# Performance work log

Hardware: AMD Instinct MI355X
Metric: run time of the kernel (lower is better)

## Reference

```python
import jax, jax.numpy as jnp
import numpy as np
from jax import lax

DEC = [256, 128, 64, 32]
INS = [512, 256, 128, 64]


def _conv2d(x, w, b, pad):
    y = lax.conv_general_dilated(x, w, (1, 1), [(pad, pad), (pad, pad)],
                                 dimension_numbers=('NCHW', 'OIHW', 'NCHW'))
    return y + b[None, :, None, None]


def _conv_transpose2d(x, w_t, b):
    # torch ConvTranspose2d(k=3, stride=2, padding=1, output_padding=1): H -> 2H
    # equivalent to lhs-dilated conv with spatially flipped, IO-transposed kernel
    w = jnp.flip(jnp.transpose(w_t, (1, 0, 2, 3)), (2, 3))  # [out, in, 3, 3]
    y = lax.conv_general_dilated(x, w, (1, 1), [(1, 2), (1, 2)],
                                 lhs_dilation=(2, 2),
                                 dimension_numbers=('NCHW', 'OIHW', 'NCHW'))
    return y + b[None, :, None, None]


def setup_inputs() -> dict:
    key = jax.random.key(0)
    ks = iter(jax.random.split(key, 40))
    d = {}
    d['enc_feat'] = jax.random.normal(next(ks), (8, 512, 16, 16), jnp.float32)
    d['semantic_map'] = jax.random.normal(next(ks), (8, 32, 256, 256), jnp.float32)

    def w(k, shape, fan_in):
        return jax.random.normal(k, shape, jnp.float32) / np.float32(np.sqrt(fan_in))

    for i in range(4):
        d['wt%d' % i] = w(next(ks), (INS[i], DEC[i], 3, 3), INS[i] * 9)  # torch convT layout [in,out,kh,kw]
        d['bt%d' % i] = jnp.zeros((DEC[i],), jnp.float32)
        d['wc%d' % i] = w(next(ks), (DEC[i], DEC[i], 3, 3), DEC[i] * 9)
        d['bc%d' % i] = jnp.zeros((DEC[i],), jnp.float32)
    d['w_attn'] = w(next(ks), (16, 32, 1, 1), 32)
    d['b_attn'] = jnp.zeros((16,), jnp.float32)
    d['w_fin'] = w(next(ks), (1, 16, 1, 1), 16)
    d['b_fin'] = jnp.zeros((1,), jnp.float32)
    return d


def _forward(enc_feat, semantic_map, wts, bts, wcs, bcs, w_attn, b_attn, w_fin, b_fin):
    x = enc_feat
    for i in range(4):
        x = jax.nn.elu(_conv_transpose2d(x, wts[i], bts[i]))
        x = jax.nn.elu(_conv2d(x, wcs[i], bcs[i], 1))
        # skip concats are zero-channel in the only executable config -> identity
    # DynamicSemanticAttention (channel attention over C' = in_ch // 2)
    q = _conv2d(x, w_attn, b_attn, 0)                 # [B, 16, H, W]
    kf = _conv2d(semantic_map, w_attn, b_attn, 0)     # [B, 16, H, W]
    B, C, H, W = q.shape
    qf = q.reshape(B, C, H * W)                        # [B, C', N]
    attn = jnp.einsum('bcn,bdn->bcd', qf, kf.reshape(B, C, H * W))  # [B, C', C']
    attn = jax.nn.softmax(attn, axis=-1)
    fused = jnp.einsum('bcd,bdn->bcn', attn, qf).reshape(B, C, H, W) + q
    return jax.nn.sigmoid(_conv2d(fused, w_fin, b_fin, 0))  # [B, 1, H, W]


def reference(enc_feat, semantic_map, wt0, bt0, wc0, bc0, wt1, bt1, wc1, bc1,
              wt2, bt2, wc2, bc2, wt3, bt3, wc3, bc3, w_attn, b_attn, w_fin, b_fin):
    wts = [wt0, wt1, wt2, wt3]
    bts = [bt0, bt1, bt2, bt3]
    wcs = [wc0, wc1, wc2, wc3]
    bcs = [bc0, bc1, bc2, bc3]
    return _forward(enc_feat, semantic_map, wts, bts, wcs, bcs,
                    w_attn, b_attn, w_fin, b_fin)
```

## Files before the change

### kernel.cpp

```cpp
#include <hip/hip_runtime.h>
#include <hip/hip_bf16.h>
#include <math.h>

typedef _Float16 f16;
typedef _Float16 h8 __attribute__((ext_vector_type(8)));
typedef _Float16 h4 __attribute__((ext_vector_type(4)));
typedef float    f4 __attribute__((ext_vector_type(4)));

__device__ __forceinline__ float elu_f(float v) { return v > 0.f ? v : __expf(v) - 1.f; }
__device__ __forceinline__ float sigmoid_f(float v) { return 1.f / (1.f + __expf(-v)); }

struct PrepDesc { const float* src; unsigned dstOff; int OC; int IC; int tr; };
struct P8 { PrepDesc d[8]; };

__global__ void prep_all_k(P8 p, f16* __restrict__ wp,
                           const float* __restrict__ enc, f16* __restrict__ enc_cl) {
    __shared__ float ts[32][257];
    if (blockIdx.x < 128) {
        const int b = blockIdx.x >> 4, cg = blockIdx.x & 15;
        const int tid = threadIdx.x;
        #pragma unroll
        for (int i = 0; i < 32; ++i)
            ts[i][tid] = enc[((size_t)(b * 512 + cg * 32 + i)) * 256 + tid];
        __syncthreads();
        #pragma unroll
        for (int k = 0; k < 4; ++k) {
            h8 v;
            #pragma unroll
            for (int q = 0; q < 8; ++q) v[q] = (f16)ts[k * 8 + q][tid];
            *(h8*)(enc_cl + ((size_t)(b * 256 + tid)) * 512 + cg * 32 + k * 8) = v;
        }
        return;
    }
    unsigned idx = (blockIdx.x - 128) * 256u + threadIdx.x;
    for (int s = 0; s < 8; ++s) {
        const int IC = p.d[s].IC, OC = p.d[s].OC;
        const unsigned cnt = (unsigned)(OC * 9 * IC);
        if (idx < cnt) {
            const int nicc = IC >> 5;
            const int j    = idx & 7;
            const int lane = (idx >> 3) & 63;
            const int mt   = (idx >> 9) & 1;
            unsigned r = idx >> 10;
            const int tap = r % 9;  r /= 9;
            const int icchunk = r % nicc;
            const int ocg     = r / nicc;
            const int oc = ocg * 32 + mt * 16 + (lane & 15);
            const int ic = icchunk * 32 + (lane >> 4) * 8 + j;
            const float v = p.d[s].tr ? p.d[s].src[((size_t)ic * OC + oc) * 9 + tap]
                                      : p.d[s].src[((size_t)oc * IC + ic) * 9 + tap];
            wp[p.d[s].dstOff + idx] = (f16)v;
            return;
        }
        idx -= cnt;
    }
}

template<int SKS>
__device__ __forceinline__ h8 stage_elem(const f16* __restrict__ in, size_t off,
                                         size_t srcTot, const float* __restrict__ sbias,
                                         int ch0) {
    if constexpr (SKS == 1) {
        return *(const h8*)(in + off);
    } else {
        float s[8];
        const h8 t0 = *(const h8*)(in + off);
        #pragma unroll
        for (int j = 0; j < 8; ++j) s[j] = (float)t0[j];
        #pragma unroll
        for (int k = 1; k < SKS; ++k) {
            const h8 tk = *(const h8*)(in + (size_t)k * srcTot + off);
            #pragma unroll
            for (int j = 0; j < 8; ++j) s[j] += (float)tk[j];
        }
        const float4 b0 = *(const float4*)(sbias + ch0);
        const float4 b1 = *(const float4*)(sbias + ch0 + 4);
        h8 v;
        v[0] = (f16)elu_f(s[0] + b0.x); v[1] = (f16)elu_f(s[1] + b0.y);
        v[2] = (f16)elu_f(s[2] + b0.z); v[3] = (f16)elu_f(s[3] + b0.w);
        v[4] = (f16)elu_f(s[4] + b1.x); v[5] = (f16)elu_f(s[5] + b1.y);
        v[6] = (f16)elu_f(s[6] + b1.z); v[7] = (f16)elu_f(s[7] + b1.w);
        return v;
    }
}

template<int C, int H, int W, int HT, int WT, int NWN, int KS, int SKS>
__launch_bounds__(256, 2)
__global__ void conv3_mfma(const f16* __restrict__ in, const f16* __restrict__ wp,
                           const float* __restrict__ bias, const float* __restrict__ sbias,
                           size_t srcTot, f16* __restrict__ out, f16* __restrict__ pout) {
    constexpr int NWR = 4 / NWN;
    constexpr int RH  = HT / NWR;
    constexpr int PIXR = WT + 2;
    constexpr int ROWS = HT + 2;
    constexpr int XB = ROWS * PIXR * 80;
    constexpr int NICC = C / 32;
    constexpr int XTILES = W / WT;
    __shared__ __align__(16) char xlds[XB];

    const int tid = threadIdx.x;
    const int wid = tid >> 6, lane = tid & 63;
    const int ln15 = lane & 15, lg = lane >> 4;
    const int ni = wid % NWN, ri = wid / NWN;
    const int bz = blockIdx.z;
    const int bb = bz / (C / 32), ocg = bz % (C / 32);
    const int oc0 = ocg * 32;
    const int bx = blockIdx.x;
    const int xt = bx % XTILES, ks = bx / XTILES;
    const int h0 = blockIdx.y * HT, w0 = xt * WT;
    const int colb = ni * 16 + ln15;

    f4 acc[RH][2] = {};

    for (int icc = ks * (C / KS); icc < (ks + 1) * (C / KS); icc += 32) {
        __syncthreads();
        for (int t = tid; t < ROWS * PIXR * 4; t += 256) {
            const int g = t & 3, pix = t >> 2;
            const int rr = pix / PIXR, ww = pix - rr * PIXR;
            const int gh = h0 - 1 + rr, gw = w0 - 1 + ww;
            h8 v = {};
            if (gh >= 0 && gh < H && gw >= 0 && gw < W) {
                const size_t off = (((size_t)bb * H + gh) * W + gw) * C + icc + g * 8;
                v = stage_elem<SKS>(in, off, srcTot, sbias, icc + g * 8);
            }
            *(h8*)(xlds + pix * 80 + g * 16) = v;
        }
        __syncthreads();

        const f16* wbl = wp + ((size_t)(ocg * NICC + (icc >> 5)) * 18) * 512 + lane * 8;
        #pragma unroll
        for (int dw = 0; dw < 3; ++dw) {
            h8 afd[3][2];
            #pragma unroll
            for (int dh = 0; dh < 3; ++dh)
                #pragma unroll
                for (int mt = 0; mt < 2; ++mt)
                    afd[dh][mt] = *(const h8*)(wbl + ((dh * 3 + dw) * 2 + mt) * 512);
            h8 bfv[RH + 2];
            #pragma unroll
            for (int q = 0; q < RH + 2; ++q)
                bfv[q] = *(const h8*)(xlds + ((ri * RH + q) * PIXR + colb + dw) * 80 + lg * 16);
            #pragma unroll
            for (int r = 0; r < RH; ++r) {
                #pragma unroll
                for (int dh = 0; dh < 3; ++dh) {
                    acc[r][0] = __builtin_amdgcn_mfma_f32_16x16x32_f16(afd[dh][0], bfv[r + dh], acc[r][0], 0, 0, 0);
                    acc[r][1] = __builtin_amdgcn_mfma_f32_16x16x32_f16(afd[dh][1], bfv[r + dh], acc[r][1], 0, 0, 0);
                }
            }
        }
    }

    #pragma unroll
    for (int r = 0; r < RH; ++r) {
        const int oh = h0 + ri * RH + r;
        const int ow = w0 + colb;
        #pragma unroll
        for (int mt = 0; mt < 2; ++mt) {
            const int ocl = mt * 16 + lg * 4;
            const f4 v = acc[r][mt];
            if constexpr (KS > 1) {
                const size_t TOT = (size_t)8 * H * W * C;
                h4 hv = {(f16)v.x, (f16)v.y, (f16)v.z, (f16)v.w};
                *(h4*)(pout + (size_t)ks * TOT +
                       (((size_t)bb * H + oh) * W + ow) * C + oc0 + ocl) = hv;
            } else {
                const float4 b4 = *(const float4*)(bias + oc0 + ocl);
                h4 hv = {(f16)elu_f(v.x + b4.x), (f16)elu_f(v.y + b4.y),
                         (f16)elu_f(v.z + b4.z), (f16)elu_f(v.w + b4.w)};
                *(h4*)(out + (((size_t)bb * H + oh) * W + ow) * C + oc0 + ocl) = hv;
            }
        }
    }
}

template<int IC, int OC, int Hi, int Wi, int KS, int SKS>
__launch_bounds__(256, 2)
__global__ void convt_mfma(const f16* __restrict__ in, const f16* __restrict__ wp,
                           const float* __restrict__ bias, const float* __restrict__ sbias,
                           size_t srcTot, f16* __restrict__ out, f16* __restrict__ pout) {
    constexpr int HT = 4, WT = 16;
    constexpr int PIXR = WT + 1;
    constexpr int ROWS = HT + 1;
    constexpr int XB = ROWS * PIXR * 80;
    constexpr int NICC = IC / 32;
    constexpr int XTILES = Wi / WT;
    __shared__ __align__(16) char xlds[XB];

    const int tid = threadIdx.x;
    const int wid = tid >> 6, lane = tid & 63;
    const int ln15 = lane & 15, lg = lane >> 4;
    const int iloc = wid;
    const int bz = blockIdx.z;
    const int bb = bz / (OC / 32), ocg = bz % (OC / 32);
    const int oc0 = ocg * 32;
    const int bx = blockIdx.x;
    const int xt = bx % XTILES, ks = bx / XTILES;
    const int i0 = blockIdx.y * HT, j0 = xt * WT;

    f4 acc[4][2] = {};

    for (int icc = ks * (IC / KS); icc < (ks + 1) * (IC / KS); icc += 32) {
        __syncthreads();
        for (int t = tid; t < ROWS * PIXR * 4; t += 256) {
            const int g = t & 3, pix = t >> 2;
            const int rr = pix / PIXR, ww = pix - rr * PIXR;
            const int gh = i0 + rr, gw = j0 + ww;
            h8 v = {};
            if (gh < Hi && gw < Wi) {
                const size_t off = (((size_t)bb * Hi + gh) * Wi + gw) * IC + icc + g * 8;
                v = stage_elem<SKS>(in, off, srcTot, sbias, icc + g * 8);
            }
            *(h8*)(xlds + pix * 80 + g * 16) = v;
        }
        __syncthreads();

        const f16* wbl = wp + ((size_t)(ocg * NICC + (icc >> 5)) * 18) * 512 + lane * 8;
        h8 af[9][2];
        #pragma unroll
        for (int tap = 0; tap < 9; ++tap)
            #pragma unroll
            for (int mt = 0; mt < 2; ++mt)
                af[tap][mt] = *(const h8*)(wbl + (tap * 2 + mt) * 512);

        h8 bf[2][2];
        #pragma unroll
        for (int a = 0; a < 2; ++a)
            #pragma unroll
            for (int b = 0; b < 2; ++b)
                bf[a][b] = *(const h8*)(xlds + ((iloc + a) * PIXR + ln15 + b) * 80 + lg * 16);

        #pragma unroll
        for (int p = 0; p < 4; ++p) {
            const int di = p >> 1, dj = p & 1;
            #pragma unroll
            for (int a = 0; a < 2; ++a) {
                if (a > di) continue;
                const int kh = 1 + di - 2 * a;
                #pragma unroll
                for (int b = 0; b < 2; ++b) {
                    if (b > dj) continue;
                    const int kw = 1 + dj - 2 * b;
                    const int tap = kh * 3 + kw;
                    acc[p][0] = __builtin_amdgcn_mfma_f32_16x16x32_f16(af[tap][0], bf[a][b], acc[p][0], 0, 0, 0);
                    acc[p][1] = __builtin_amdgcn_mfma_f32_16x16x32_f16(af[tap][1], bf[a][b], acc[p][1], 0, 0, 0);
                }
            }
        }
    }

    #pragma unroll
    for (int p = 0; p < 4; ++p) {
        const int orow = 2 * (i0 + iloc) + (p >> 1);
        const int ocol = 2 * (j0 + ln15) + (p & 1);
        #pragma unroll
        for (int mt = 0; mt < 2; ++mt) {
            const int ocl = mt * 16 + lg * 4;
            const f4 v = acc[p][mt];
            if constexpr (KS > 1) {
                const size_t TOT = (size_t)8 * (2 * Hi) * (2 * Wi) * OC;
                h4 hv = {(f16)v.x, (f16)v.y, (f16)v.z, (f16)v.w};
                *(h4*)(pout + (size_t)ks * TOT +
                       (((size_t)bb * (2 * Hi) + orow) * (2 * Wi) + ocol) * OC + oc0 + ocl) = hv;
            } else {
                const float4 b4 = *(const float4*)(bias + oc0 + ocl);
                h4 hv = {(f16)elu_f(v.x + b4.x), (f16)elu_f(v.y + b4.y),
                         (f16)elu_f(v.z + b4.z), (f16)elu_f(v.w + b4.w)};
                *(h4*)(out + (((size_t)bb * (2 * Hi) + orow) * (2 * Wi) + ocol) * OC + oc0 + ocl) = hv;
            }
        }
    }
}

#define KCH 128
__launch_bounds__(256)
__global__ void gram_mfma_k(const f16* __restrict__ x3, const float* __restrict__ sem,
                            float* __restrict__ part, float* __restrict__ sums) {
    __shared__ __align__(16) f16 xs[4][32][66];
    __shared__ float pl[4][1024];
    __shared__ float sl[4][64];
    const int b = blockIdx.y, kc = blockIdx.x;
    const int tid = threadIdx.x, wid = tid >> 6, lane = tid & 63;
    const int row = lane & 15, kg = lane >> 4;
    const size_t N = 65536;
    const int p0 = kc * 512 + wid * 128;

    const float* sb = sem + ((size_t)b * 32 + row) * N + p0 + kg * 8;
    const int spx = lane >> 1, shalf = lane & 1;

    f4 acc00 = {}, acc01 = {}, acc10 = {}, acc11 = {};
    float sx0 = 0.f, sx1 = 0.f, ss0 = 0.f, ss1 = 0.f;

    for (int s = 0; s < 4; ++s) {
        const f16* xp = x3 + ((size_t)b * N + p0 + s * 32 + spx) * 32 + shalf * 16;
        const h8 w0 = *(const h8*)xp;
        const h8 w1 = *(const h8*)(xp + 8);
        const float4 f0 = *(const float4*)(sb + s * 32);
        const float4 f1 = *(const float4*)(sb + s * 32 + 4);
        const float4 g0 = *(const float4*)(sb + 16 * N + s * 32);
        const float4 g1 = *(const float4*)(sb + 16 * N + s * 32 + 4);
        *(h8*)&xs[wid][spx][shalf * 16]     = w0;
        *(h8*)&xs[wid][spx][shalf * 16 + 8] = w1;
        h8 a0, a1;
        #pragma unroll
        for (int j = 0; j < 8; ++j) {
            a0[j] = xs[wid][kg * 8 + j][row];
            a1[j] = xs[wid][kg * 8 + j][row + 16];
        }
        const h8 b0 = {(f16)f0.x, (f16)f0.y, (f16)f0.z, (f16)f0.w,
                       (f16)f1.x, (f16)f1.y, (f16)f1.z, (f16)f1.w};
        const h8 b1 = {(f16)g0.x, (f16)g0.y, (f16)g0.z, (f16)g0.w,
                       (f16)g1.x, (f16)g1.y, (f16)g1.z, (f16)g1.w};
        acc00 = __builtin_amdgcn_mfma_f32_16x16x32_f16(a0, b0, acc00, 0, 0, 0);
        acc01 = __builtin_amdgcn_mfma_f32_16x16x32_f16(a0, b1, acc01, 0, 0, 0);
        acc10 = __builtin_amdgcn_mfma_f32_16x16x32_f16(a1, b0, acc10, 0, 0, 0);
        acc11 = __builtin_amdgcn_mfma_f32_16x16x32_f16(a1, b1, acc11, 0, 0, 0);
        #pragma unroll
        for (int q = 0; q < 8; ++q) { sx0 += (float)a0[q]; sx1 += (float)a1[q]; }
        ss0 += (f0.x + f0.y + f0.z + f0.w) + (f1.x + f1.y + f1.z + f1.w);
        ss1 += (g0.x + g0.y + g0.z + g0.w) + (g1.x + g1.y + g1.z + g1.w);
    }

    sx0 += __shfl_xor(sx0, 16); sx0 += __shfl_xor(sx0, 32);
    sx1 += __shfl_xor(sx1, 16); sx1 += __shfl_xor(sx1, 32);
    ss0 += __shfl_xor(ss0, 16); ss0 += __shfl_xor(ss0, 32);
    ss1 += __shfl_xor(ss1, 16); ss1 += __shfl_xor(ss1, 32);

    #pragma unroll
    for (int reg = 0; reg < 4; ++reg) {
        const int c0 = 4 * kg + reg;
        pl[wid][c0 * 32 + row]               = acc00[reg];
        pl[wid][c0 * 32 + 16 + row]          = acc01[reg];
        pl[wid][(16 + c0) * 32 + row]        = acc10[reg];
        pl[wid][(16 + c0) * 32 + 16 + row]   = acc11[reg];
    }
    if (lane < 16) {
        sl[wid][row]      = sx0;
        sl[wid][16 + row] = sx1;
        sl[wid][32 + row] = ss0;
        sl[wid][48 + row] = ss1;
    }
    __syncthreads();

    float* pb = part + ((size_t)b * KCH + kc) * 1024;
    #pragma unroll
    for (int t = tid; t < 1024; t += 256)
        pb[t] = pl[0][t] + pl[1][t] + pl[2][t] + pl[3][t];
    if (tid < 64)
        sums[((size_t)b * KCH + kc) * 64 + tid] = sl[0][tid] + sl[1][tid] + sl[2][tid] + sl[3][tid];
}

__launch_bounds__(256)
__global__ void gram_reduce_k(const float* __restrict__ part, const float* __restrict__ sums,
                              float* __restrict__ part2, float* __restrict__ sums2) {
    const int b = blockIdx.y, g = blockIdx.x;
    const int tid = threadIdx.x;
    const int i4 = tid * 4;
    f4 a = {};
    #pragma unroll 4
    for (int ch = 0; ch < 16; ++ch) {
        const f4 v = *(const f4*)(part + ((size_t)b * KCH + g * 16 + ch) * 1024 + i4);
        a.x += v.x; a.y += v.y; a.z += v.z; a.w += v.w;
    }
    *(f4*)(part2 + ((size_t)b * 8 + g) * 1024 + i4) = a;
    if (tid < 64) {
        float s = 0.f;
        #pragma unroll 4
        for (int ch = 0; ch < 16; ++ch) s += sums[((size_t)b * KCH + g * 16 + ch) * 64 + tid];
        sums2[((size_t)b * 8 + g) * 64 + tid] = s;
    }
}

__launch_bounds__(256)
__global__ void attn_finish_v3(const float* __restrict__ part, const float* __restrict__ sums,
                               const float* __restrict__ wa, const float* __restrict__ ba,
                               const float* __restrict__ wf, const float* __restrict__ bf,
                               float* __restrict__ u, float* __restrict__ cb) {
    __shared__ float G[32][33];
    __shared__ float T[16][33];
    __shared__ float A[16][17];
    __shared__ float Sx[32], Ss[32], px[16], ps[16], v[16];
    const int b = blockIdx.x, tid = threadIdx.x;

    float a4[4] = {0.f, 0.f, 0.f, 0.f};
    for (int p = 0; p < 8; ++p) {
        const float* pp = part + ((size_t)b * 8 + p) * 1024 + tid;
        a4[0] += pp[0]; a4[1] += pp[256]; a4[2] += pp[512]; a4[3] += pp[768];
    }
    #pragma unroll
    for (int q = 0; q < 4; ++q) {
        const int t = tid + q * 256;
        G[t >> 5][t & 31] = a4[q];
    }
    if (tid < 64) {
        float s = 0.f;
        for (int p = 0; p < 8; ++p) s += sums[((size_t)b * 8 + p) * 64 + tid];
        if (tid < 32) Sx[tid] = s; else Ss[tid - 32] = s;
    }
    __syncthreads();
    for (int t = tid; t < 512; t += 256) {
        const int c = t >> 5, f = t & 31;
        float s = 0.f;
        #pragma unroll
        for (int e = 0; e < 32; ++e) s = fmaf(wa[c * 32 + e], G[e][f], s);
        T[c][f] = s;
    }
    if (tid < 32) {
        const int c = tid & 15;
        const float* S = (tid < 16) ? Sx : Ss;
        float s = 0.f;
        #pragma unroll
        for (int e = 0; e < 32; ++e) s = fmaf(wa[c * 32 + e], S[e], s);
        if (tid < 16) px[c] = s; else ps[c] = s;
    }
    __syncthreads();
    {
        const int c = tid >> 4, d = tid & 15;
        float s = 0.f;
        #pragma unroll
        for (int f2 = 0; f2 < 32; ++f2) s = fmaf(T[c][f2], wa[d * 32 + f2], s);
        s += px[c] * ba[d] + ba[c] * ps[d] + 65536.f * ba[c] * ba[d];
        A[c][d] = s;
    }
    __syncthreads();
    if (tid < 16) {
        float m = A[tid][0];
        #pragma unroll
        for (int d = 1; d < 16; ++d) m = fmaxf(m, A[tid][d]);
        float s = 0.f;
        #pragma unroll
        for (int d = 0; d < 16; ++d) { const float e = __expf(A[tid][d] - m); A[tid][d] = e; s += e; }
        const float inv = 1.f / s;
        #pragma unroll
        for (int d = 0; d < 16; ++d) A[tid][d] *= inv;
    }
    __syncthreads();
    if (tid < 16) {
        float s = wf[tid];
        #pragma unroll
        for (int c = 0; c < 16; ++c) s = fmaf(wf[c], A[c][tid], s);
        v[tid] = s;
    }
    __syncthreads();
    if (tid < 32) {
        float s = 0.f;
        #pragma unroll
        for (int d = 0; d < 16; ++d) s = fmaf(v[d], wa[d * 32 + tid], s);
        u[b * 32 + tid] = s;
    }
    if (tid == 0) {
        float s2 = bf[0];
        #pragma unroll
        for (int d = 0; d < 16; ++d) s2 = fmaf(v[d], ba[d], s2);
        cb[b] = s2;
    }
}

__launch_bounds__(256)
__global__ void final_k(const f16* __restrict__ x3, const float* __restrict__ u,
                        const float* __restrict__ cb, float* __restrict__ out) {
    const int b = blockIdx.y;
    const int nn = blockIdx.x * 256 + threadIdx.x;
    const f16* xb = x3 + ((size_t)b * 65536 + nn) * 32;
    const float* ub = u + b * 32;
    float acc = cb[b];
    #pragma unroll
    for (int g = 0; g < 4; ++g) {
        const h8 v = *(const h8*)(xb + g * 8);
        #pragma unroll
        for (int q = 0; q < 8; ++q) acc = fmaf(ub[g * 8 + q], (float)v[q], acc);
    }
    out[(size_t)b * 65536 + nn] = sigmoid_f(acc);
}

extern "C" void kernel_launch(void* const* d_in, const int* in_sizes, int n_in,
                              void* d_out, int out_size, void* d_ws, size_t ws_size,
                              hipStream_t stream) {
    const float* enc   = (const float*)d_in[0];
    const float* sem   = (const float*)d_in[1];
    const float* wt0   = (const float*)d_in[2];
    const float* bt0   = (const float*)d_in[3];
    const float* wc0   = (const float*)d_in[4];
    const float* bc0   = (const float*)d_in[5];
    const float* wt1   = (const float*)d_in[6];
    const float* bt1   = (const float*)d_in[7];
    const float* wc1   = (const float*)d_in[8];
    const float* bc1   = (const float*)d_in[9];
    const float* wt2   = (const float*)d_in[10];
    const float* bt2   = (const float*)d_in[11];
    const float* wc2   = (const float*)d_in[12];
    const float* bc2   = (const float*)d_in[13];
    const float* wt3   = (const float*)d_in[14];
    const float* bt3   = (const float*)d_in[15];
    const float* wc3   = (const float*)d_in[16];
    const float* bc3   = (const float*)d_in[17];
    const float* wattn = (const float*)d_in[18];
    const float* battn = (const float*)d_in[19];
    const float* wfin  = (const float*)d_in[20];
    const float* bfin  = (const float*)d_in[21];

    char* W = (char*)d_ws;
    f16*   actA   = (f16*)(W + 0);
    f16*   actB   = (f16*)(W + 33554432);
    f16*   x3cl   = (f16*)(W + 67108864);
    f16*   wp     = (f16*)(W + 100663296);
    f16*   enc_cl = (f16*)(W + 105906176);
    float* part   = (float*)(W + 108003328);
    float* sums   = (float*)(W + 112197632);
    float* part2  = (float*)(W + 112459776);
    float* sums2  = (float*)(W + 112721920);
    float* u      = (float*)(W + 112738304);
    float* cb     = (float*)(W + 112739328);
    float* out    = (float*)d_out;
    f16* pfA = actA;
    f16* pfB = actB;

    P8 p;
    p.d[0] = {wt0, 0u,       256, 512, 1};
    p.d[1] = {wc0, 1179648u, 256, 256, 0};
    p.d[2] = {wt1, 1769472u, 128, 256, 1};
    p.d[3] = {wc1, 2064384u, 128, 128, 0};
    p.d[4] = {wt2, 2211840u,  64, 128, 1};
    p.d[5] = {wc2, 2285568u,  64,  64, 0};
    p.d[6] = {wt3, 2322432u,  32,  64, 1};
    p.d[7] = {wc3, 2340864u,  32,  32, 0};
    prep_all_k<<<9308, 256, 0, stream>>>(p, wp, enc, enc_cl);

    convt_mfma<512, 256, 16, 16, 4, 1><<<dim3(4, 4, 64), 256, 0, stream>>>(
        enc_cl, wp, nullptr, nullptr, 0, nullptr, pfA);
    conv3_mfma<256, 32, 32, 8, 32, 2, 4, 4><<<dim3(4, 4, 64), 256, 0, stream>>>(
        pfA, wp + 1179648, nullptr, bt0, 2097152, nullptr, pfB);
    convt_mfma<256, 128, 32, 32, 2, 4><<<dim3(4, 8, 32), 256, 0, stream>>>(
        pfB, wp + 1769472, nullptr, bc0, 2097152, nullptr, pfA);
    conv3_mfma<128, 64, 64, 4, 64, 4, 2, 2><<<dim3(2, 16, 32), 256, 0, stream>>>(
        pfA, wp + 2064384, nullptr, bt1, 4194304, nullptr, pfB);
    convt_mfma<128, 64, 64, 64, 1, 2><<<dim3(4, 16, 16), 256, 0, stream>>>(
        pfB, wp + 2211840, bt2, bc1, 4194304, actA, nullptr);
    conv3_mfma<64, 128, 128, 4, 64, 4, 1, 1><<<dim3(2, 32, 16), 256, 0, stream>>>(
        actA, wp + 2285568, bc2, nullptr, 0, actB, nullptr);
    convt_mfma<64, 32, 128, 128, 1, 1><<<dim3(8, 32, 8), 256, 0, stream>>>(
        actB, wp + 2322432, bt3, nullptr, 0, actA, nullptr);
    conv3_mfma<32, 256, 256, 4, 64, 4, 1, 1><<<dim3(4, 64, 8), 256, 0, stream>>>(
        actA, wp + 2340864, bc3, nullptr, 0, x3cl, nullptr);

    gram_mfma_k<<<dim3(KCH, 8), 256, 0, stream>>>(x3cl, sem, part, sums);
    gram_reduce_k<<<dim3(8, 8), 256, 0, stream>>>(part, sums, part2, sums2);
    attn_finish_v3<<<8, 256, 0, stream>>>(part2, sums2, wattn, battn, wfin, bfin, u, cb);
    final_k<<<dim3(256, 8), 256, 0, stream>>>(x3cl, u, cb, out);
}
```

Baseline: 227.7 us.

## Fuse final conv3 with gram accumulation and retune early decoder split-K

The last 3x3 conv (32 channels, 256x256) now also computes the per-tile gram partials and row sums against the semantic map, using the freshly computed activations kept in LDS. This removes the separate gram kernel and its reread of x3 from global memory. The partial count doubles to 256 chunks per batch, so the reduce kernel reads more data. The early decoder stages also get new conv3/convt template parameters and split-K factors, and the bias/ELU epilogues move to different stages.

Result: no change. 228.7 us (+0.4%).

```diff
diff --git a/kernel.cpp b/kernel.cpp
--- a/kernel.cpp
+++ b/kernel.cpp
@@ -272,53 +272,116 @@
     }
 }
 
-#define KCH 128
-__launch_bounds__(256)
-__global__ void gram_mfma_k(const f16* __restrict__ x3, const float* __restrict__ sem,
-                            float* __restrict__ part, float* __restrict__ sums) {
-    __shared__ __align__(16) f16 xs[4][32][66];
-    __shared__ float pl[4][1024];
-    __shared__ float sl[4][64];
-    const int b = blockIdx.y, kc = blockIdx.x;
-    const int tid = threadIdx.x, wid = tid >> 6, lane = tid & 63;
-    const int row = lane & 15, kg = lane >> 4;
+__launch_bounds__(256, 2)
+__global__ void conv3_gram_k(const f16* __restrict__ in, const f16* __restrict__ wp,
+                             const float* __restrict__ bias, const float* __restrict__ sem,
+                             f16* __restrict__ out, float* __restrict__ part,
+                             float* __restrict__ sums) {
+    constexpr int C = 32, H = 256, W = 256, HT = 4, WT = 64;
+    constexpr int PIXR = WT + 2;
+    constexpr int ROWS = HT + 2;
+    constexpr int XB = ROWS * PIXR * 80;
+    constexpr int X3B = 32 * 264 * 2;
+    constexpr int LDSB = X3B + 16384 + 1024;
+    __shared__ __align__(16) char lds[(XB > LDSB) ? XB : LDSB];
+    char* xlds = lds;
+    f16*   x3l = (f16*)lds;
+    float* pl  = (float*)(lds + X3B);
+    float* sl  = (float*)(lds + X3B + 16384);
+
+    const int tid = threadIdx.x;
+    const int wid = tid >> 6, lane = tid & 63;
+    const int ln15 = lane & 15, lg = lane >> 4;
+    const int ni = wid;
+    const int bb = blockIdx.z;
+    const int h0 = blockIdx.y * HT, w0 = blockIdx.x * WT;
+    const int colb = ni * 16 + ln15;
+
+    f4 acc[4][2] = {};
+
+    for (int t = tid; t < ROWS * PIXR * 4; t += 256) {
+        const int g = t & 3, pix = t >> 2;
+        const int rr = pix / PIXR, ww = pix - rr * PIXR;
+        const int gh = h0 - 1 + rr, gw = w0 - 1 + ww;
+        h8 v = {};
+        if (gh >= 0 && gh < H && gw >= 0 && gw < W)
+            v = *(const h8*)(in + (((size_t)bb * H + gh) * W + gw) * C + g * 8);
+        *(h8*)(xlds + pix * 80 + g * 16) = v;
+    }
+    __syncthreads();
+
+    const f16* wbl = wp + lane * 8;
+    #pragma unroll
+    for (int dw = 0; dw < 3; ++dw) {
+        h8 afd[3][2];
+        #pragma unroll
+        for (int dh = 0; dh < 3; ++dh)
+            #pragma unroll
+            for (int mt = 0; mt < 2; ++mt)
+                afd[dh][mt] = *(const h8*)(wbl + ((dh * 3 + dw) * 2 + mt) * 512);
+        h8 bfv[6];
+        #pragma unroll
+        for (int q = 0; q < 6; ++q)
+            bfv[q] = *(const h8*)(xlds + (q * PIXR + colb + dw) * 80 + lg * 16);
+        #pragma unroll
+        for (int r = 0; r < 4; ++r) {
+            #pragma unroll
+            for (int dh = 0; dh < 3; ++dh) {
+                acc[r][0] = __builtin_amdgcn_mfma_f32_16x16x32_f16(afd[dh][0], bfv[r + dh], acc[r][0], 0, 0, 0);
+                acc[r][1] = __builtin_amdgcn_mfma_f32_16x16x32_f16(afd[dh][1], bfv[r + dh], acc[r][1], 0, 0, 0);
+            }
+        }
+    }
+    __syncthreads();
+
+    #pragma unroll
+    for (int r = 0; r < 4; ++r) {
+        const int oh = h0 + r, ow = w0 + colb;
+        const int px = r * 64 + colb;
+        #pragma unroll
+        for (int mt = 0; mt < 2; ++mt) {
+            const int ocl = mt * 16 + lg * 4;
+            const float4 b4 = *(const float4*)(bias + ocl);
+            const f4 v = acc[r][mt];
+            h4 hv = {(f16)elu_f(v.x + b4.x), (f16)elu_f(v.y + b4.y),
+                     (f16)elu_f(v.z + b4.z), (f16)elu_f(v.w + b4.w)};
+            *(h4*)(out + (((size_t)bb * H + oh) * W + ow) * C + ocl) = hv;
+            x3l[(ocl + 0) * 264 + px] = hv[0];
+            x3l[(ocl + 1) * 264 + px] = hv[1];
+            x3l[(ocl + 2) * 264 + px] = hv[2];
+            x3l[(ocl + 3) * 264 + px] = hv[3];
+        }
+    }
+    __syncthreads();
+
+    const int row = ln15, kg = lg;
     const size_t N = 65536;
-    const int p0 = kc * 512 + wid * 128;
-
-    const float* sb = sem + ((size_t)b * 32 + row) * N + p0 + kg * 8;
-    const int spx = lane >> 1, shalf = lane & 1;
-
-    f4 acc00 = {}, acc01 = {}, acc10 = {}, acc11 = {};
+    const float* sb = sem + ((size_t)bb * 32 + row) * N + (size_t)(h0 + wid) * 256 + w0 + kg * 8;
+
+    f4 g00 = {}, g01 = {}, g10 = {}, g11 = {};
     float sx0 = 0.f, sx1 = 0.f, ss0 = 0.f, ss1 = 0.f;
 
-    for (int s = 0; s < 4; ++s) {
-        const f16* xp = x3 + ((size_t)b * N + p0 + s * 32 + spx) * 32 + shalf * 16;
-        const h8 w0 = *(const h8*)xp;
-        const h8 w1 = *(const h8*)(xp + 8);
-        const float4 f0 = *(const float4*)(sb + s * 32);
-        const float4 f1 = *(const float4*)(sb + s * 32 + 4);
-        const float4 g0 = *(const float4*)(sb + 16 * N + s * 32);
-        const float4 g1 = *(const float4*)(sb + 16 * N + s * 32 + 4);
-        *(h8*)&xs[wid][spx][shalf * 16]     = w0;
-        *(h8*)&xs[wid][spx][shalf * 16 + 8] = w1;
-        h8 a0, a1;
-        #pragma unroll
-        for (int j = 0; j < 8; ++j) {
-            a0[j] = xs[wid][kg * 8 + j][row];
-            a1[j] = xs[wid][kg * 8 + j][row + 16];
-        }
+    #pragma unroll
+    for (int ks = 0; ks < 2; ++ks) {
+        const int k0 = ks * 32;
+        const h8 a0 = *(const h8*)(x3l + row * 264 + wid * 64 + k0 + kg * 8);
+        const h8 a1 = *(const h8*)(x3l + (row + 16) * 264 + wid * 64 + k0 + kg * 8);
+        const float4 f0 = *(const float4*)(sb + k0);
+        const float4 f1 = *(const float4*)(sb + k0 + 4);
+        const float4 q0 = *(const float4*)(sb + 16 * N + k0);
+        const float4 q1 = *(const float4*)(sb + 16 * N + k0 + 4);
         const h8 b0 = {(f16)f0.x, (f16)f0.y, (f16)f0.z, (f16)f0.w,
                        (f16)f1.x, (f16)f1.y, (f16)f1.z, (f16)f1.w};
-        const h8 b1 = {(f16)g0.x, (f16)g0.y, (f16)g0.z, (f16)g0.w,
-                       (f16)g1.x, (f16)g1.y, (f16)g1.z, (f16)g1.w};
-        acc00 = __builtin_amdgcn_mfma_f32_16x16x32_f16(a0, b0, acc00, 0, 0, 0);
-        acc01 = __builtin_amdgcn_mfma_f32_16x16x32_f16(a0, b1, acc01, 0, 0, 0);
-        acc10 = __builtin_amdgcn_mfma_f32_16x16x32_f16(a1, b0, acc10, 0, 0, 0);
-        acc11 = __builtin_amdgcn_mfma_f32_16x16x32_f16(a1, b1, acc11, 0, 0, 0);
+        const h8 b1 = {(f16)q0.x, (f16)q0.y, (f16)q0.z, (f16)q0.w,
+                       (f16)q1.x, (f16)q1.y, (f16)q1.z, (f16)q1.w};
+        g00 = __builtin_amdgcn_mfma_f32_16x16x32_f16(a0, b0, g00, 0, 0, 0);
+        g01 = __builtin_amdgcn_mfma_f32_16x16x32_f16(a0, b1, g01, 0, 0, 0);
+        g10 = __builtin_amdgcn_mfma_f32_16x16x32_f16(a1, b0, g10, 0, 0, 0);
+        g11 = __builtin_amdgcn_mfma_f32_16x16x32_f16(a1, b1, g11, 0, 0, 0);
         #pragma unroll
         for (int q = 0; q < 8; ++q) { sx0 += (float)a0[q]; sx1 += (float)a1[q]; }
         ss0 += (f0.x + f0.y + f0.z + f0.w) + (f1.x + f1.y + f1.z + f1.w);
-        ss1 += (g0.x + g0.y + g0.z + g0.w) + (g1.x + g1.y + g1.z + g1.w);
+        ss1 += (q0.x + q0.y + q0.z + q0.w) + (q1.x + q1.y + q1.z + q1.w);
     }
 
     sx0 += __shfl_xor(sx0, 16); sx0 += __shfl_xor(sx0, 32);
@@ -329,25 +392,25 @@
     #pragma unroll
     for (int reg = 0; reg < 4; ++reg) {
         const int c0 = 4 * kg + reg;
-        pl[wid][c0 * 32 + row]               = acc00[reg];
-        pl[wid][c0 * 32 + 16 + row]          = acc01[reg];
-        pl[wid][(16 + c0) * 32 + row]        = acc10[reg];
-        pl[wid][(16 + c0) * 32 + 16 + row]   = acc11[reg];
+        pl[wid * 1024 + c0 * 32 + row]             = g00[reg];
+        pl[wid * 1024 + c0 * 32 + 16 + row]        = g01[reg];
+        pl[wid * 1024 + (16 + c0) * 32 + row]      = g10[reg];
+        pl[wid * 1024 + (16 + c0) * 32 + 16 + row] = g11[reg];
     }
     if (lane < 16) {
-        sl[wid][row]      = sx0;
-        sl[wid][16 + row] = sx1;
-        sl[wid][32 + row] = ss0;
-        sl[wid][48 + row] = ss1;
-    }
-    __syncthreads();
-
-    float* pb = part + ((size_t)b * KCH + kc) * 1024;
-    #pragma unroll
+        sl[wid * 64 + row]      = sx0;
+        sl[wid * 64 + 16 + row] = sx1;
+        sl[wid * 64 + 32 + row] = ss0;
+        sl[wid * 64 + 48 + row] = ss1;
+    }
+    __syncthreads();
+
+    const int chunk = blockIdx.y * 4 + blockIdx.x;
+    float* pb = part + ((size_t)bb * 256 + chunk) * 1024;
     for (int t = tid; t < 1024; t += 256)
-        pb[t] = pl[0][t] + pl[1][t] + pl[2][t] + pl[3][t];
+        pb[t] = pl[t] + pl[1024 + t] + pl[2048 + t] + pl[3072 + t];
     if (tid < 64)
-        sums[((size_t)b * KCH + kc) * 64 + tid] = sl[0][tid] + sl[1][tid] + sl[2][tid] + sl[3][tid];
+        sums[((size_t)bb * 256 + chunk) * 64 + tid] = sl[tid] + sl[64 + tid] + sl[128 + tid] + sl[192 + tid];
 }
 
 __launch_bounds__(256)
@@ -358,15 +421,15 @@
     const int i4 = tid * 4;
     f4 a = {};
     #pragma unroll 4
-    for (int ch = 0; ch < 16; ++ch) {
-        const f4 v = *(const f4*)(part + ((size_t)b * KCH + g * 16 + ch) * 1024 + i4);
+    for (int ch = 0; ch < 32; ++ch) {
+        const f4 v = *(const f4*)(part + ((size_t)b * 256 + g * 32 + ch) * 1024 + i4);
         a.x += v.x; a.y += v.y; a.z += v.z; a.w += v.w;
     }
     *(f4*)(part2 + ((size_t)b * 8 + g) * 1024 + i4) = a;
     if (tid < 64) {
         float s = 0.f;
         #pragma unroll 4
-        for (int ch = 0; ch < 16; ++ch) s += sums[((size_t)b * KCH + g * 16 + ch) * 64 + tid];
+        for (int ch = 0; ch < 32; ++ch) s += sums[((size_t)b * 256 + g * 32 + ch) * 64 + tid];
         sums2[((size_t)b * 8 + g) * 64 + tid] = s;
     }
 }
@@ -506,14 +569,13 @@
     f16*   wp     = (f16*)(W + 100663296);
     f16*   enc_cl = (f16*)(W + 105906176);
     float* part   = (float*)(W + 108003328);
-    float* sums   = (float*)(W + 112197632);
-    float* part2  = (float*)(W + 112459776);
-    float* sums2  = (float*)(W + 112721920);
-    float* u      = (float*)(W + 112738304);
-    float* cb     = (float*)(W + 112739328);
+    float* sums   = (float*)(W + 116391936);
+    float* part2  = (float*)(W + 116916224);
+    float* sums2  = (float*)(W + 117178368);
+    float* u      = (float*)(W + 117194752);
+    float* cb     = (float*)(W + 117195776);
     float* out    = (float*)d_out;
     f16* pfA = actA;
-    f16* pfB = actB;
 
     P8 p;
     p.d[0] = {wt0, 0u,       256, 512, 1};
@@ -528,22 +590,21 @@
 
     convt_mfma<512, 256, 16, 16, 4, 1><<<dim3(4, 4, 64), 256, 0, stream>>>(
         enc_cl, wp, nullptr, nullptr, 0, nullptr, pfA);
-    conv3_mfma<256, 32, 32, 8, 32, 2, 4, 4><<<dim3(4, 4, 64), 256, 0, stream>>>(
-        pfA, wp + 1179648, nullptr, bt0, 2097152, nullptr, pfB);
-    convt_mfma<256, 128, 32, 32, 2, 4><<<dim3(4, 8, 32), 256, 0, stream>>>(
-        pfB, wp + 1769472, nullptr, bc0, 2097152, nullptr, pfA);
-    conv3_mfma<128, 64, 64, 4, 64, 4, 2, 2><<<dim3(2, 16, 32), 256, 0, stream>>>(
-        pfA, wp + 2064384, nullptr, bt1, 4194304, nullptr, pfB);
-    convt_mfma<128, 64, 64, 64, 1, 2><<<dim3(4, 16, 16), 256, 0, stream>>>(
-        pfB, wp + 2211840, bt2, bc1, 4194304, actA, nullptr);
+    conv3_mfma<256, 32, 32, 4, 16, 1, 1, 4><<<dim3(2, 8, 64), 256, 0, stream>>>(
+        pfA, wp + 1179648, bc0, bt0, 2097152, actB, nullptr);
+    convt_mfma<256, 128, 32, 32, 2, 1><<<dim3(4, 8, 32), 256, 0, stream>>>(
+        actB, wp + 1769472, nullptr, nullptr, 0, nullptr, pfA);
+    conv3_mfma<128, 64, 64, 4, 32, 2, 1, 2><<<dim3(2, 16, 32), 256, 0, stream>>>(
+        pfA, wp + 2064384, bc1, bt1, 4194304, actB, nullptr);
+    convt_mfma<128, 64, 64, 64, 1, 1><<<dim3(4, 16, 16), 256, 0, stream>>>(
+        actB, wp + 2211840, bt2, nullptr, 0, actA, nullptr);
     conv3_mfma<64, 128, 128, 4, 64, 4, 1, 1><<<dim3(2, 32, 16), 256, 0, stream>>>(
         actA, wp + 2285568, bc2, nullptr, 0, actB, nullptr);
     convt_mfma<64, 32, 128, 128, 1, 1><<<dim3(8, 32, 8), 256, 0, stream>>>(
         actB, wp + 2322432, bt3, nullptr, 0, actA, nullptr);
-    conv3_mfma<32, 256, 256, 4, 64, 4, 1, 1><<<dim3(4, 64, 8), 256, 0, stream>>>(
-        actA, wp + 2340864, bc3, nullptr, 0, x3cl, nullptr);
-
-    gram_mfma_k<<<dim3(KCH, 8), 256, 0, stream>>>(x3cl, sem, part, sums);
+    conv3_gram_k<<<dim3(4, 64, 8), 256, 0, stream>>>(
+        actA, wp + 2340864, bc3, sem, x3cl, part, sums);
+
     gram_reduce_k<<<dim3(8, 8), 256, 0, stream>>>(part, sums, part2, sums2);
     attn_finish_v3<<<8, 256, 0, stream>>>(part2, sums2, wattn, battn, wfin, bfin, u, cb);
     final_k<<<dim3(256, 8), 256, 0, stream>>>(x3cl, u, cb, out);
```
